# Kernel optimization log

Measured on AMD Instinct MI355X. Metric: run time of the kernel, lower is better.

## Reference

```python
import jax, jax.numpy as jnp
import numpy as np

# Graph sizes
B, N, E = 8, 512, 262144          # graphs, nodes/graph, total edges
ND, ED, GD = 128, 64, 32          # node, edge, glob feature dims
FIN = 2 * ND + ED                 # 320 = msg('sr') + existing edges
CTX = GD                          # ctxt_dim = 0, ctxt is globs only
H1, OUT = 256, 64                 # feat_net hidden / output (== ED for 'add' residual)
AH, NHEADS = 64, 4                # attn_net hidden / heads
HEAD = OUT // NHEADS              # 16
EPS = 1e-5


def setup_inputs() -> dict:
    key = jax.random.key(0)
    ks = jax.random.split(key, 12)
    nodes = jax.random.normal(ks[0], (B, N, ND), jnp.float32)
    edges0 = jax.random.normal(ks[1], (E, ED), jnp.float32)
    globs = jax.random.normal(ks[2], (B, GD), jnp.float32)
    batch_idx = jnp.sort(jax.random.randint(ks[3], (E,), 0, B, jnp.int32))
    send_idx = jax.random.randint(ks[4], (E,), 0, N, jnp.int32)
    recv_idx = jax.random.randint(ks[5], (E,), 0, N, jnp.int32)
    # LayerNorm params over feat_inpt_dim
    ln_g = jnp.ones((FIN,), jnp.float32)
    ln_b = jnp.zeros((FIN,), jnp.float32)
    # feat_net: 2-layer SiLU MLP, ctxt concatenated at the input
    W1 = 0.05 * jax.random.normal(ks[6], (FIN + CTX, H1), jnp.float32)
    b1 = jnp.zeros((H1,), jnp.float32)
    W2 = 0.05 * jax.random.normal(ks[7], (H1, OUT), jnp.float32)
    b2 = jnp.zeros((OUT,), jnp.float32)
    # attn_net: 2-layer SiLU MLP -> n_heads scores
    A1 = 0.05 * jax.random.normal(ks[8], (FIN + CTX, AH), jnp.float32)
    ab1 = jnp.zeros((AH,), jnp.float32)
    A2 = 0.05 * jax.random.normal(ks[9], (AH, NHEADS), jnp.float32)
    ab2 = jnp.zeros((NHEADS,), jnp.float32)
    return dict(nodes=nodes, edges0=edges0, globs=globs, ln_g=ln_g, ln_b=ln_b,
                W1=W1, b1=b1, W2=W2, b2=b2, A1=A1, ab1=ab1, A2=A2, ab2=ab2,
                batch_idx=batch_idx, send_idx=send_idx, recv_idx=recv_idx)


def reference(nodes, edges0, globs, ln_g, ln_b, W1, b1, W2, b2, A1, ab1, A2, ab2,
              batch_idx, send_idx, recv_idx):
    # Build messages: gather sender/receiver node feats per edge ('sr')
    send = nodes[batch_idx, send_idx]                      # [E, ND]
    recv = nodes[batch_idx, recv_idx]                      # [E, ND]
    feats = jnp.concatenate([edges0, send, recv], axis=-1)  # [E, FIN]
    # Pre-LN
    mu = feats.mean(-1, keepdims=True)
    var = feats.var(-1, keepdims=True)
    feats = (feats - mu) * jax.lax.rsqrt(var + EPS) * ln_g + ln_b
    # Broadcast per-graph globals to edges (ctxt_from_mask)
    x = jnp.concatenate([feats, globs[batch_idx]], axis=-1)  # [E, FIN+CTX]
    # Attention scores / sqrt(feat_outp_dim)
    a = (jax.nn.silu(x @ A1 + ab1) @ A2 + ab2) / np.sqrt(OUT)  # [E, NHEADS]
    # Segment softmax over the sender dim (group by (graph, receiver))
    seg = batch_idx * N + recv_idx
    nseg = B * N
    amax = jax.ops.segment_max(a, seg, num_segments=nseg)
    amax = jnp.where(jnp.isfinite(amax), amax, 0.0)
    ae = jnp.exp(a - amax[seg])
    denom = jax.ops.segment_sum(ae, seg, num_segments=nseg)
    attn = ae / denom[seg]                                  # [E, NHEADS]
    attn = jnp.repeat(attn, HEAD, axis=-1)                  # [E, OUT]
    # Edge feature update + additive residual
    new_edges = jax.nn.silu(x @ W1 + b1) @ W2 + b2 + edges0  # [E, OUT]
    # Attention-weighted scatter-sum pool over senders, zeros for isolated nodes
    pooled = jax.ops.segment_sum(new_edges * attn, seg, num_segments=nseg)
    pooled = pooled.reshape(B, N, OUT)
    return new_edges, pooled
```

## Files before the change

### kernel.cpp

```cpp
#include <hip/hip_runtime.h>
#include <hip/hip_bf16.h>
#include <cstdint>

typedef __bf16 bf16;
typedef __bf16 bf16x8 __attribute__((ext_vector_type(8)));
typedef float f32x4 __attribute__((ext_vector_type(4)));

#define E_TOT   262144
#define NNODE   512
#define NDIM    128
#define EDIM    64
#define GDIM    32
#define FIN     320
#define XD      352
#define H1D     256
#define OUTD    64
#define AHD     64
#define NHEADS  4
#define NSEG    4096
#define TE      48

#define SX_STR  360
#define SH_STR  264
#define SA_STR  72

#define PRM_LNG 0
#define PRM_LNB 320
#define PRM_B1  640
#define PRM_B2  896
#define PRM_A2  960
#define PRM_AB1 1216
#define PRM_AB2 1280
#define PRM_TOT 1284

#define SMEM_SX    0
#define SMEM_SA    25600
#define SMEM_SCORE 34560
#define SMEM_A2    35328
#define SMEM_LNG   36352
#define SMEM_LNB   37632
#define SMEM_IDX   38912
#define SMEM_TOT   39680

__device__ __forceinline__ float siluf(float v) {
    return v / (1.0f + __expf(-v));
}

__device__ __forceinline__ bool probe_bf16(const void* nodes, int t) {
    const unsigned short* u16 = (const unsigned short*)nodes;
    int lane = t & 63;
    int pl = 0;
    #pragma unroll
    for (int i = 0; i < 4; i++) {
        unsigned short u = u16[lane * 4 + i];
        int expo = (u >> 7) & 0xFF;
        pl += (((u & 0x7FFF) == 0) || (expo >= 97 && expo <= 137)) ? 1 : 0;
    }
    #pragma unroll
    for (int m = 1; m < 64; m <<= 1) pl += __shfl_xor(pl, m);
    return pl >= 240;
}

__global__ __launch_bounds__(256) void k_prep(
    const void* __restrict__ nodes,
    const void* __restrict__ W1, const void* __restrict__ W2, const void* __restrict__ A1,
    const void* __restrict__ ln_g, const void* __restrict__ ln_b,
    const void* __restrict__ b1, const void* __restrict__ b2,
    const void* __restrict__ A2, const void* __restrict__ ab1, const void* __restrict__ ab2,
    bf16* __restrict__ W1T, bf16* __restrict__ W2T, bf16* __restrict__ A1T,
    float* __restrict__ prm) {
    int b = blockIdx.x, t = threadIdx.x;
    bool isb = probe_bf16(nodes, t);
    if (b < 352) {
        int i = b * 256 + t;
        int k = i / H1D, n = i % H1D;
        float v = isb ? (float)((const bf16*)W1)[i] : ((const float*)W1)[i];
        W1T[n * XD + k] = (bf16)v;
    } else if (b < 416) {
        int i = (b - 352) * 256 + t;
        int k = i / OUTD, n = i % OUTD;
        float v = isb ? (float)((const bf16*)W2)[i] : ((const float*)W2)[i];
        W2T[n * H1D + k] = (bf16)v;
    } else if (b < 504) {
        int i = (b - 416) * 256 + t;
        int k = i / AHD, n = i % AHD;
        float v = isb ? (float)((const bf16*)A1)[i] : ((const float*)A1)[i];
        A1T[n * XD + k] = (bf16)v;
    } else {
        int i = (b - 504) * 256 + t;
        if (i < PRM_TOT) {
            const void* src; int off;
            if (i < 320)       { src = ln_g; off = i; }
            else if (i < 640)  { src = ln_b; off = i - 320; }
            else if (i < 896)  { src = b1;   off = i - 640; }
            else if (i < 960)  { src = b2;   off = i - 896; }
            else if (i < 1216) { src = A2;   off = i - 960; }
            else if (i < 1280) { src = ab1;  off = i - 1216; }
            else               { src = ab2;  off = i - 1280; }
            prm[i] = isb ? (float)((const bf16*)src)[off] : ((const float*)src)[off];
        }
    }
}

__global__ __launch_bounds__(256, 4) void k_edge(
    const void* __restrict__ nodes, const void* __restrict__ edges0,
    const void* __restrict__ globs, const float* __restrict__ prm,
    const int* __restrict__ bidx, const int* __restrict__ sidx,
    const int* __restrict__ ridx,
    const bf16* __restrict__ W1T, const bf16* __restrict__ W2T,
    const bf16* __restrict__ A1T,
    void* __restrict__ outNE, float* __restrict__ denom,
    float* __restrict__ pooled) {

    __shared__ __align__(16) char smem[SMEM_TOT];
    bf16*  sX    = (bf16*)(smem + SMEM_SX);
    bf16*  sH    = (bf16*)(smem + SMEM_SX);
    bf16*  sA    = (bf16*)(smem + SMEM_SA);
    float* sScore= (float*)(smem + SMEM_SCORE);
    float* sA2   = (float*)(smem + SMEM_A2);
    float* sLnG  = (float*)(smem + SMEM_LNG);
    float* sLnB  = (float*)(smem + SMEM_LNB);
    int*   sBi   = (int*)(smem + SMEM_IDX);
    int*   sSi   = sBi + TE;
    int*   sRi   = sBi + 2 * TE;
    int*   sSeg  = sBi + 3 * TE;

    const int t  = threadIdx.x;
    const int e0 = blockIdx.x * TE;
    const int ne = min(TE, E_TOT - e0);
    const bool isb = probe_bf16(nodes, t);

    if (t < TE) {
        int ge = e0 + t;
        if (t < ne) {
            int bi = bidx[ge], si = sidx[ge], ri = ridx[ge];
            sBi[t] = bi; sSi[t] = si; sRi[t] = ri;
            sSeg[t] = bi * NNODE + ri;
        } else {
            sBi[t] = 0; sSi[t] = 0; sRi[t] = 0; sSeg[t] = 0;
        }
    } else if (t < 128) {
        int c = t - 48;
        if (c < 80) ((float4*)sLnG)[c] = ((const float4*)(prm + PRM_LNG))[c];
    } else if (t < 208) {
        int c = t - 128;
        ((float4*)sLnB)[c] = ((const float4*)(prm + PRM_LNB))[c];
    } else {
        int c = t - 208;
        if (c < 32) {
            ((float4*)sA2)[c]      = ((const float4*)(prm + PRM_A2))[c];
            ((float4*)sA2)[c + 32] = ((const float4*)(prm + PRM_A2))[c + 32];
        }
    }
    __syncthreads();

    {
        const int eh = t >> 3, gl = t & 7;
        for (int half = 0; half < 2; half++) {
            const int e = half * 32 + eh;
            if (e >= TE) break;
            if (e >= ne) {
                bf16x8 zz = {};
                #pragma unroll
                for (int j = 0; j < 6; j++) {
                    int c = gl + j * 8;
                    if (c < 44) *(bf16x8*)&sX[e * SX_STR + c * 8] = zz;
                }
                continue;
            }
            const int ge = e0 + e;
            const int bi = sBi[e], si = sSi[e], ri = sRi[e];
            float v[40];
            #pragma unroll
            for (int j = 0; j < 5; j++) {
                const int c = gl + j * 8;
                const void* base; size_t off;
                if (c < 8)       { base = edges0; off = (size_t)ge * EDIM + c * 8; }
                else if (c < 24) { base = nodes;  off = (size_t)(bi * NNODE + si) * NDIM + (c - 8) * 8; }
                else             { base = nodes;  off = (size_t)(bi * NNODE + ri) * NDIM + (c - 24) * 8; }
                if (isb) {
                    bf16x8 x = *(const bf16x8*)((const bf16*)base + off);
                    #pragma unroll
                    for (int ii = 0; ii < 8; ii++) v[j * 8 + ii] = (float)x[ii];
                } else {
                    const float* sf = (const float*)base + off;
                    float4 f0 = ((const float4*)sf)[0];
                    float4 f1 = ((const float4*)sf)[1];
                    v[j*8+0]=f0.x; v[j*8+1]=f0.y; v[j*8+2]=f0.z; v[j*8+3]=f0.w;
                    v[j*8+4]=f1.x; v[j*8+5]=f1.y; v[j*8+6]=f1.z; v[j*8+7]=f1.w;
                }
            }
            float s = 0.f, sq = 0.f;
            #pragma unroll
            for (int ii = 0; ii < 40; ii++) { s += v[ii]; sq += v[ii] * v[ii]; }
            #pragma unroll
            for (int m = 1; m < 8; m <<= 1) { s += __shfl_xor(s, m); sq += __shfl_xor(sq, m); }
            float mean = s * (1.0f / FIN);
            float var  = sq * (1.0f / FIN) - mean * mean;
            float rstd = rsqrtf(var + 1e-5f);
            #pragma unroll
            for (int j = 0; j < 5; j++) {
                const int c = gl + j * 8;
                const float* gP = &sLnG[c * 8];
                const float* bP = &sLnB[c * 8];
                bf16x8 o;
                #pragma unroll
                for (int ii = 0; ii < 8; ii++)
                    o[ii] = (bf16)((v[j * 8 + ii] - mean) * rstd * gP[ii] + bP[ii]);
                *(bf16x8*)&sX[e * SX_STR + c * 8] = o;
            }
            if (gl < 4) {
                const int c = 40 + gl;
                size_t off = (size_t)bi * GDIM + gl * 8;
                bf16x8 o;
                if (isb) {
                    o = *(const bf16x8*)((const bf16*)globs + off);
                } else {
                    const float* sf = (const float*)globs + off;
                    float4 f0 = ((const float4*)sf)[0];
                    float4 f1 = ((const float4*)sf)[1];
                    o[0]=(bf16)f0.x; o[1]=(bf16)f0.y; o[2]=(bf16)f0.z; o[3]=(bf16)f0.w;
                    o[4]=(bf16)f1.x; o[5]=(bf16)f1.y; o[6]=(bf16)f1.z; o[7]=(bf16)f1.w;
                }
                *(bf16x8*)&sX[e * SX_STR + c * 8] = o;
            }
        }
    }
    __syncthreads();

    const int w = t >> 6, lane = t & 63, quad = lane >> 4, l15 = lane & 15;
    f32x4 z = {0.f, 0.f, 0.f, 0.f};

    f32x4 acc[3][4], accA[3];
    #pragma unroll
    for (int s2 = 0; s2 < 3; s2++) { accA[s2] = z; for (int i = 0; i < 4; i++) acc[s2][i] = z; }
    {
        const bf16* pW = W1T + (size_t)(w * 64 + l15) * XD + quad * 8;
        const bf16* pA = A1T + (size_t)(w * 16 + l15) * XD + quad * 8;
        bf16x8 bw[4], ba;
        #pragma unroll
        for (int i = 0; i < 4; i++) bw[i] = *(const bf16x8*)(pW + (size_t)i * 16 * XD);
        ba = *(const bf16x8*)pA;
        for (int kk = 0; kk < 11; kk++) {
            bf16x8 bwn[4], ban;
            if (kk < 10) {
                #pragma unroll
                for (int i = 0; i < 4; i++) bwn[i] = *(const bf16x8*)(pW + (size_t)i * 16 * XD + (kk + 1) * 32);
                ban = *(const bf16x8*)(pA + (kk + 1) * 32);
            }
            const int kc = kk * 32 + quad * 8;
            bf16x8 a[3];
            #pragma unroll
            for (int s2 = 0; s2 < 3; s2++) a[s2] = *(bf16x8*)&sX[(s2 * 16 + l15) * SX_STR + kc];
            #pragma unroll
            for (int i = 0; i < 4; i++)
                #pragma unroll
                for (int s2 = 0; s2 < 3; s2++)
                    acc[s2][i] = __builtin_amdgcn_mfma_f32_16x16x32_bf16(a[s2], bw[i], acc[s2][i], 0, 0, 0);
            #pragma unroll
            for (int s2 = 0; s2 < 3; s2++)
                accA[s2] = __builtin_amdgcn_mfma_f32_16x16x32_bf16(a[s2], ba, accA[s2], 0, 0, 0);
            if (kk < 10) {
                #pragma unroll
                for (int i = 0; i < 4; i++) bw[i] = bwn[i];
                ba = ban;
            }
        }
    }
    __syncthreads();

    #pragma unroll
    for (int i = 0; i < 4; i++) {
        const int n = w * 64 + i * 16 + l15;
        const float bb = prm[PRM_B1 + n];
        #pragma unroll
        for (int s2 = 0; s2 < 3; s2++)
            #pragma unroll
            for (int r = 0; r < 4; r++)
                sH[(s2 * 16 + quad * 4 + r) * SH_STR + n] = (bf16)siluf(acc[s2][i][r] + bb);
    }
    {
        const int n = w * 16 + l15;
        const float ba1 = prm[PRM_AB1 + n];
        #pragma unroll
        for (int s2 = 0; s2 < 3; s2++)
            #pragma unroll
            for (int r = 0; r < 4; r++)
                sA[(s2 * 16 + quad * 4 + r) * SA_STR + n] = (bf16)siluf(accA[s2][r] + ba1);
    }
    __syncthreads();

    if (t < TE * NHEADS) {
        const int e = t >> 2, h = t & 3;
        if (e < ne) {
            float dot = 0.f;
            #pragma unroll
            for (int c = 0; c < 8; c++) {
                bf16x8 v = *(bf16x8*)&sA[e * SA_STR + c * 8];
                #pragma unroll
                for (int ii = 0; ii < 8; ii++)
                    dot += (float)v[ii] * sA2[(c * 8 + ii) * NHEADS + h];
            }
            float ex = __expf((dot + prm[PRM_AB2 + h]) * 0.125f);
            sScore[e * 4 + h] = ex;
            atomicAdd(&denom[sSeg[e] * NHEADS + h], ex);
        }
    }
    __syncthreads();

    {
        f32x4 c2[3] = {z, z, z};
        const int n = w * 16 + l15;
        const bf16* pW2 = W2T + (size_t)n * H1D + quad * 8;
        bf16x8 b2f = *(const bf16x8*)pW2;
        for (int kk = 0; kk < 8; kk++) {
            bf16x8 b2n;
            if (kk < 7) b2n = *(const bf16x8*)(pW2 + (kk + 1) * 32);
            const int kc = kk * 32 + quad * 8;
            #pragma unroll
            for (int s2 = 0; s2 < 3; s2++) {
                bf16x8 a = *(bf16x8*)&sH[(s2 * 16 + l15) * SH_STR + kc];
                c2[s2] = __builtin_amdgcn_mfma_f32_16x16x32_bf16(a, b2f, c2[s2], 0, 0, 0);
            }
            if (kk < 7) b2f = b2n;
        }
        const float bb2 = prm[PRM_B2 + n];
        #pragma unroll
        for (int s2 = 0; s2 < 3; s2++)
            #pragma unroll
            for (int r = 0; r < 4; r++) {
                const int row = s2 * 16 + quad * 4 + r;
                if (row < ne) {
                    size_t off = (size_t)(e0 + row) * EDIM + n;
                    float ev = isb ? (float)((const bf16*)edges0)[off] : ((const float*)edges0)[off];
                    float v = c2[s2][r] + bb2 + ev;
                    if (isb) ((bf16*)outNE)[off] = (bf16)v;
                    else     ((float*)outNE)[off] = v;
                    float ex = sScore[row * 4 + w];
                    atomicAdd(&pooled[(size_t)sSeg[row] * OUTD + n], v * ex);
                }
            }
    }
}

__global__ __launch_bounds__(256) void k_norm(const float* __restrict__ pooled,
                                              const float* __restrict__ denom,
                                              const void* __restrict__ nodes,
                                              void* __restrict__ d_out) {
    int i = blockIdx.x * 256 + threadIdx.x;
    bool isb = probe_bf16(nodes, threadIdx.x);
    int s = i >> 6, j = i & 63, h = j >> 4;
    float den = denom[s * 4 + h];
    float v = (den > 0.f) ? pooled[i] / den : 0.0f;
    size_t po = (size_t)E_TOT * OUTD + i;
    if (isb) ((bf16*)d_out)[po] = (bf16)v;
    else     ((float*)d_out)[po] = v;
}

static char* align_up(char* p, size_t a) {
    return (char*)(((uintptr_t)p + (a - 1)) & ~(uintptr_t)(a - 1));
}

extern "C" void kernel_launch(void* const* d_in, const int* in_sizes, int n_in,
                              void* d_out, int out_size, void* d_ws, size_t ws_size,
                              hipStream_t stream) {
    const void* nodes  = d_in[0];
    const void* edges0 = d_in[1];
    const void* globs  = d_in[2];
    const void* ln_g   = d_in[3];
    const void* ln_b   = d_in[4];
    const void* W1     = d_in[5];
    const void* b1     = d_in[6];
    const void* W2     = d_in[7];
    const void* b2     = d_in[8];
    const void* A1     = d_in[9];
    const void* ab1    = d_in[10];
    const void* A2     = d_in[11];
    const void* ab2    = d_in[12];
    const int*  bidx   = (const int*)d_in[13];
    const int*  sidx   = (const int*)d_in[14];
    const int*  ridx   = (const int*)d_in[15];

    char* p = (char*)d_ws;
    float*    prm    = (float*)p;    p = align_up(p + PRM_TOT * 4, 256);
    bf16*     W1T    = (bf16*)p;     p = align_up(p + XD * H1D * 2, 256);
    bf16*     W2T    = (bf16*)p;     p = align_up(p + H1D * OUTD * 2, 256);
    bf16*     A1T    = (bf16*)p;     p = align_up(p + XD * AHD * 2, 256);
    float*    denom  = (float*)p;    p += NSEG * NHEADS * 4;
    float*    pooled = (float*)p;    p += (size_t)NSEG * OUTD * 4;

    hipMemsetAsync(denom, 0, NSEG * NHEADS * 4 + (size_t)NSEG * OUTD * 4, stream);
    k_prep<<<dim3(510), dim3(256), 0, stream>>>(
        nodes, W1, W2, A1, ln_g, ln_b, b1, b2, A2, ab1, ab2,
        W1T, W2T, A1T, prm);
    k_edge<<<dim3((E_TOT + TE - 1) / TE), dim3(256), 0, stream>>>(
        nodes, edges0, globs, prm,
        bidx, sidx, ridx, W1T, W2T, A1T, d_out, denom, pooled);
    k_norm<<<dim3(NSEG * OUTD / 256), dim3(256), 0, stream>>>(pooled, denom, nodes, d_out);
}
```

Baseline: 345.6 us.

## Shrink edge tile to 32, raise occupancy, fold zeroing into prep kernel

Reduces the edges per block from 48 to 32, which shrinks shared memory and lets the launch bound ask for 6 blocks per CU. Each thread now handles exactly one edge row in the gather/LayerNorm stage, and LN gamma/beta are read straight from global memory instead of being staged in shared memory. The memset is replaced by zeroing blocks appended to the prep kernel, MFMA loops drop their manual register prefetch and are wrapped in s_setprio, and the denominator atomics are moved to the end of the kernel. The trade-off is more blocks, with weights reloaded from global/L2 for each smaller tile, and the loss of the software prefetch.

New measurement: 385.8 us. 1.12x slower.

```diff
diff --git a/kernel.cpp b/kernel.cpp
--- a/kernel.cpp
+++ b/kernel.cpp
@@ -18,7 +18,7 @@
 #define AHD     64
 #define NHEADS  4
 #define NSEG    4096
-#define TE      48
+#define TE      32
 
 #define SX_STR  360
 #define SH_STR  264
@@ -34,16 +34,17 @@
 #define PRM_TOT 1284
 
 #define SMEM_SX    0
-#define SMEM_SA    25600
-#define SMEM_SCORE 34560
-#define SMEM_A2    35328
-#define SMEM_LNG   36352
-#define SMEM_LNB   37632
-#define SMEM_IDX   38912
-#define SMEM_TOT   39680
+#define SMEM_SA    16896
+#define SMEM_SCORE 23040
+#define SMEM_A2    23552
+#define SMEM_SEG   24576
+#define SMEM_TOT   24704
+
+#define ZOFF 510
+#define ZBLK 272
 
 __device__ __forceinline__ float siluf(float v) {
-    return v / (1.0f + __expf(-v));
+    return v * __builtin_amdgcn_rcpf(1.0f + __expf(-v));
 }
 
 __device__ __forceinline__ bool probe_bf16(const void* nodes, int t) {
@@ -68,8 +69,13 @@
     const void* __restrict__ b1, const void* __restrict__ b2,
     const void* __restrict__ A2, const void* __restrict__ ab1, const void* __restrict__ ab2,
     bf16* __restrict__ W1T, bf16* __restrict__ W2T, bf16* __restrict__ A1T,
-    float* __restrict__ prm) {
+    float* __restrict__ prm, float* __restrict__ denom) {
     int b = blockIdx.x, t = threadIdx.x;
+    if (b >= ZOFF) {
+        float4 z4 = {0.f, 0.f, 0.f, 0.f};
+        ((float4*)denom)[(b - ZOFF) * 256 + t] = z4;
+        return;
+    }
     bool isb = probe_bf16(nodes, t);
     if (b < 352) {
         int i = b * 256 + t;
@@ -102,7 +108,7 @@
     }
 }
 
-__global__ __launch_bounds__(256, 4) void k_edge(
+__global__ __launch_bounds__(256, 6) void k_edge(
     const void* __restrict__ nodes, const void* __restrict__ edges0,
     const void* __restrict__ globs, const float* __restrict__ prm,
     const int* __restrict__ bidx, const int* __restrict__ sidx,
@@ -118,112 +124,75 @@
     bf16*  sA    = (bf16*)(smem + SMEM_SA);
     float* sScore= (float*)(smem + SMEM_SCORE);
     float* sA2   = (float*)(smem + SMEM_A2);
-    float* sLnG  = (float*)(smem + SMEM_LNG);
-    float* sLnB  = (float*)(smem + SMEM_LNB);
-    int*   sBi   = (int*)(smem + SMEM_IDX);
-    int*   sSi   = sBi + TE;
-    int*   sRi   = sBi + 2 * TE;
-    int*   sSeg  = sBi + 3 * TE;
+    int*   sSeg  = (int*)(smem + SMEM_SEG);
 
     const int t  = threadIdx.x;
     const int e0 = blockIdx.x * TE;
-    const int ne = min(TE, E_TOT - e0);
     const bool isb = probe_bf16(nodes, t);
 
-    if (t < TE) {
-        int ge = e0 + t;
-        if (t < ne) {
-            int bi = bidx[ge], si = sidx[ge], ri = ridx[ge];
-            sBi[t] = bi; sSi[t] = si; sRi[t] = ri;
-            sSeg[t] = bi * NNODE + ri;
-        } else {
-            sBi[t] = 0; sSi[t] = 0; sRi[t] = 0; sSeg[t] = 0;
-        }
-    } else if (t < 128) {
-        int c = t - 48;
-        if (c < 80) ((float4*)sLnG)[c] = ((const float4*)(prm + PRM_LNG))[c];
-    } else if (t < 208) {
-        int c = t - 128;
-        ((float4*)sLnB)[c] = ((const float4*)(prm + PRM_LNB))[c];
-    } else {
-        int c = t - 208;
-        if (c < 32) {
-            ((float4*)sA2)[c]      = ((const float4*)(prm + PRM_A2))[c];
-            ((float4*)sA2)[c + 32] = ((const float4*)(prm + PRM_A2))[c + 32];
-        }
-    }
-    __syncthreads();
-
     {
+        if (t < 64) ((float4*)sA2)[t] = ((const float4*)(prm + PRM_A2))[t];
         const int eh = t >> 3, gl = t & 7;
-        for (int half = 0; half < 2; half++) {
-            const int e = half * 32 + eh;
-            if (e >= TE) break;
-            if (e >= ne) {
-                bf16x8 zz = {};
+        const int ge = e0 + eh;
+        const int bi = bidx[ge], si = sidx[ge], ri = ridx[ge];
+        if (gl == 0) sSeg[eh] = bi * NNODE + ri;
+        float v[40];
+        #pragma unroll
+        for (int j = 0; j < 5; j++) {
+            const int c = gl + j * 8;
+            const void* base; size_t off;
+            if (c < 8)       { base = edges0; off = (size_t)ge * EDIM + c * 8; }
+            else if (c < 24) { base = nodes;  off = (size_t)(bi * NNODE + si) * NDIM + (c - 8) * 8; }
+            else             { base = nodes;  off = (size_t)(bi * NNODE + ri) * NDIM + (c - 24) * 8; }
+            if (isb) {
+                bf16x8 x = *(const bf16x8*)((const bf16*)base + off);
                 #pragma unroll
-                for (int j = 0; j < 6; j++) {
-                    int c = gl + j * 8;
-                    if (c < 44) *(bf16x8*)&sX[e * SX_STR + c * 8] = zz;
-                }
-                continue;
-            }
-            const int ge = e0 + e;
-            const int bi = sBi[e], si = sSi[e], ri = sRi[e];
-            float v[40];
-            #pragma unroll
-            for (int j = 0; j < 5; j++) {
-                const int c = gl + j * 8;
-                const void* base; size_t off;
-                if (c < 8)       { base = edges0; off = (size_t)ge * EDIM + c * 8; }
-                else if (c < 24) { base = nodes;  off = (size_t)(bi * NNODE + si) * NDIM + (c - 8) * 8; }
-                else             { base = nodes;  off = (size_t)(bi * NNODE + ri) * NDIM + (c - 24) * 8; }
-                if (isb) {
-                    bf16x8 x = *(const bf16x8*)((const bf16*)base + off);
-                    #pragma unroll
-                    for (int ii = 0; ii < 8; ii++) v[j * 8 + ii] = (float)x[ii];
-                } else {
-                    const float* sf = (const float*)base + off;
-                    float4 f0 = ((const float4*)sf)[0];
-                    float4 f1 = ((const float4*)sf)[1];
-                    v[j*8+0]=f0.x; v[j*8+1]=f0.y; v[j*8+2]=f0.z; v[j*8+3]=f0.w;
-                    v[j*8+4]=f1.x; v[j*8+5]=f1.y; v[j*8+6]=f1.z; v[j*8+7]=f1.w;
-                }
-            }
-            float s = 0.f, sq = 0.f;
-            #pragma unroll
-            for (int ii = 0; ii < 40; ii++) { s += v[ii]; sq += v[ii] * v[ii]; }
-            #pragma unroll
-            for (int m = 1; m < 8; m <<= 1) { s += __shfl_xor(s, m); sq += __shfl_xor(sq, m); }
-            float mean = s * (1.0f / FIN);
-            float var  = sq * (1.0f / FIN) - mean * mean;
-            float rstd = rsqrtf(var + 1e-5f);
-            #pragma unroll
-            for (int j = 0; j < 5; j++) {
-                const int c = gl + j * 8;
-                const float* gP = &sLnG[c * 8];
-                const float* bP = &sLnB[c * 8];
-                bf16x8 o;
-                #pragma unroll
-                for (int ii = 0; ii < 8; ii++)
-                    o[ii] = (bf16)((v[j * 8 + ii] - mean) * rstd * gP[ii] + bP[ii]);
-                *(bf16x8*)&sX[e * SX_STR + c * 8] = o;
-            }
-            if (gl < 4) {
-                const int c = 40 + gl;
-                size_t off = (size_t)bi * GDIM + gl * 8;
-                bf16x8 o;
-                if (isb) {
-                    o = *(const bf16x8*)((const bf16*)globs + off);
-                } else {
-                    const float* sf = (const float*)globs + off;
-                    float4 f0 = ((const float4*)sf)[0];
-                    float4 f1 = ((const float4*)sf)[1];
-                    o[0]=(bf16)f0.x; o[1]=(bf16)f0.y; o[2]=(bf16)f0.z; o[3]=(bf16)f0.w;
-                    o[4]=(bf16)f1.x; o[5]=(bf16)f1.y; o[6]=(bf16)f1.z; o[7]=(bf16)f1.w;
-                }
-                *(bf16x8*)&sX[e * SX_STR + c * 8] = o;
-            }
+                for (int ii = 0; ii < 8; ii++) v[j * 8 + ii] = (float)x[ii];
+            } else {
+                const float* sf = (const float*)base + off;
+                float4 f0 = ((const float4*)sf)[0];
+                float4 f1 = ((const float4*)sf)[1];
+                v[j*8+0]=f0.x; v[j*8+1]=f0.y; v[j*8+2]=f0.z; v[j*8+3]=f0.w;
+                v[j*8+4]=f1.x; v[j*8+5]=f1.y; v[j*8+6]=f1.z; v[j*8+7]=f1.w;
+            }
+        }
+        float s = 0.f, sq = 0.f;
+        #pragma unroll
+        for (int ii = 0; ii < 40; ii++) { s += v[ii]; sq += v[ii] * v[ii]; }
+        #pragma unroll
+        for (int m = 1; m < 8; m <<= 1) { s += __shfl_xor(s, m); sq += __shfl_xor(sq, m); }
+        float mean = s * (1.0f / FIN);
+        float var  = sq * (1.0f / FIN) - mean * mean;
+        float rstd = rsqrtf(var + 1e-5f);
+        #pragma unroll
+        for (int j = 0; j < 5; j++) {
+            const int c = gl + j * 8;
+            float4 g0 = ((const float4*)(prm + PRM_LNG))[c * 2];
+            float4 g1 = ((const float4*)(prm + PRM_LNG))[c * 2 + 1];
+            float4 p0 = ((const float4*)(prm + PRM_LNB))[c * 2];
+            float4 p1 = ((const float4*)(prm + PRM_LNB))[c * 2 + 1];
+            float gg[8] = {g0.x, g0.y, g0.z, g0.w, g1.x, g1.y, g1.z, g1.w};
+            float pp[8] = {p0.x, p0.y, p0.z, p0.w, p1.x, p1.y, p1.z, p1.w};
+            bf16x8 o;
+            #pragma unroll
+            for (int ii = 0; ii < 8; ii++)
+                o[ii] = (bf16)((v[j * 8 + ii] - mean) * rstd * gg[ii] + pp[ii]);
+            *(bf16x8*)&sX[eh * SX_STR + c * 8] = o;
+        }
+        if (gl < 4) {
+            const int c = 40 + gl;
+            size_t off = (size_t)bi * GDIM + gl * 8;
+            bf16x8 o;
+            if (isb) {
+                o = *(const bf16x8*)((const bf16*)globs + off);
+            } else {
+                const float* sf = (const float*)globs + off;
+                float4 f0 = ((const float4*)sf)[0];
+                float4 f1 = ((const float4*)sf)[1];
+                o[0]=(bf16)f0.x; o[1]=(bf16)f0.y; o[2]=(bf16)f0.z; o[3]=(bf16)f0.w;
+                o[4]=(bf16)f1.x; o[5]=(bf16)f1.y; o[6]=(bf16)f1.z; o[7]=(bf16)f1.w;
+            }
+            *(bf16x8*)&sX[eh * SX_STR + c * 8] = o;
         }
     }
     __syncthreads();
@@ -231,40 +200,30 @@
     const int w = t >> 6, lane = t & 63, quad = lane >> 4, l15 = lane & 15;
     f32x4 z = {0.f, 0.f, 0.f, 0.f};
 
-    f32x4 acc[3][4], accA[3];
+    f32x4 acc[2][4], accA[2];
     #pragma unroll
-    for (int s2 = 0; s2 < 3; s2++) { accA[s2] = z; for (int i = 0; i < 4; i++) acc[s2][i] = z; }
+    for (int s2 = 0; s2 < 2; s2++) { accA[s2] = z; for (int i = 0; i < 4; i++) acc[s2][i] = z; }
     {
         const bf16* pW = W1T + (size_t)(w * 64 + l15) * XD + quad * 8;
         const bf16* pA = A1T + (size_t)(w * 16 + l15) * XD + quad * 8;
-        bf16x8 bw[4], ba;
-        #pragma unroll
-        for (int i = 0; i < 4; i++) bw[i] = *(const bf16x8*)(pW + (size_t)i * 16 * XD);
-        ba = *(const bf16x8*)pA;
         for (int kk = 0; kk < 11; kk++) {
-            bf16x8 bwn[4], ban;
-            if (kk < 10) {
-                #pragma unroll
-                for (int i = 0; i < 4; i++) bwn[i] = *(const bf16x8*)(pW + (size_t)i * 16 * XD + (kk + 1) * 32);
-                ban = *(const bf16x8*)(pA + (kk + 1) * 32);
-            }
+            bf16x8 bw[4], ba;
+            #pragma unroll
+            for (int i = 0; i < 4; i++)
+                bw[i] = *(const bf16x8*)(pW + (size_t)i * 16 * XD + kk * 32);
+            ba = *(const bf16x8*)(pA + kk * 32);
             const int kc = kk * 32 + quad * 8;
-            bf16x8 a[3];
-            #pragma unroll
-            for (int s2 = 0; s2 < 3; s2++) a[s2] = *(bf16x8*)&sX[(s2 * 16 + l15) * SX_STR + kc];
-            #pragma unroll
-            for (int i = 0; i < 4; i++)
-                #pragma unroll
-                for (int s2 = 0; s2 < 3; s2++)
-                    acc[s2][i] = __builtin_amdgcn_mfma_f32_16x16x32_bf16(a[s2], bw[i], acc[s2][i], 0, 0, 0);
-            #pragma unroll
-            for (int s2 = 0; s2 < 3; s2++)
-                accA[s2] = __builtin_amdgcn_mfma_f32_16x16x32_bf16(a[s2], ba, accA[s2], 0, 0, 0);
-            if (kk < 10) {
-                #pragma unroll
-                for (int i = 0; i < 4; i++) bw[i] = bwn[i];
-                ba = ban;
-            }
+            bf16x8 a0 = *(bf16x8*)&sX[l15 * SX_STR + kc];
+            bf16x8 a1 = *(bf16x8*)&sX[(16 + l15) * SX_STR + kc];
+            __builtin_amdgcn_s_setprio(1);
+            #pragma unroll
+            for (int i = 0; i < 4; i++) {
+                acc[0][i] = __builtin_amdgcn_mfma_f32_16x16x32_bf16(a0, bw[i], acc[0][i], 0, 0, 0);
+                acc[1][i] = __builtin_amdgcn_mfma_f32_16x16x32_bf16(a1, bw[i], acc[1][i], 0, 0, 0);
+            }
+            accA[0] = __builtin_amdgcn_mfma_f32_16x16x32_bf16(a0, ba, accA[0], 0, 0, 0);
+            accA[1] = __builtin_amdgcn_mfma_f32_16x16x32_bf16(a1, ba, accA[1], 0, 0, 0);
+            __builtin_amdgcn_s_setprio(0);
         }
     }
     __syncthreads();
@@ -274,7 +233,7 @@
         const int n = w * 64 + i * 16 + l15;
         const float bb = prm[PRM_B1 + n];
         #pragma unroll
-        for (int s2 = 0; s2 < 3; s2++)
+        for (int s2 = 0; s2 < 2; s2++)
             #pragma unroll
             for (int r = 0; r < 4; r++)
                 sH[(s2 * 16 + quad * 4 + r) * SH_STR + n] = (bf16)siluf(acc[s2][i][r] + bb);
@@ -283,7 +242,7 @@
         const int n = w * 16 + l15;
         const float ba1 = prm[PRM_AB1 + n];
         #pragma unroll
-        for (int s2 = 0; s2 < 3; s2++)
+        for (int s2 = 0; s2 < 2; s2++)
             #pragma unroll
             for (int r = 0; r < 4; r++)
                 sA[(s2 * 16 + quad * 4 + r) * SA_STR + n] = (bf16)siluf(accA[s2][r] + ba1);
@@ -292,54 +251,57 @@
 
     if (t < TE * NHEADS) {
         const int e = t >> 2, h = t & 3;
-        if (e < ne) {
-            float dot = 0.f;
-            #pragma unroll
-            for (int c = 0; c < 8; c++) {
-                bf16x8 v = *(bf16x8*)&sA[e * SA_STR + c * 8];
-                #pragma unroll
-                for (int ii = 0; ii < 8; ii++)
-                    dot += (float)v[ii] * sA2[(c * 8 + ii) * NHEADS + h];
-            }
-            float ex = __expf((dot + prm[PRM_AB2 + h]) * 0.125f);
-            sScore[e * 4 + h] = ex;
-            atomicAdd(&denom[sSeg[e] * NHEADS + h], ex);
-        }
+        float dot = 0.f;
+        #pragma unroll
+        for (int c = 0; c < 8; c++) {
+            bf16x8 vv = *(bf16x8*)&sA[e * SA_STR + c * 8];
+            #pragma unroll
+            for (int ii = 0; ii < 8; ii++)
+                dot += (float)vv[ii] * sA2[(c * 8 + ii) * NHEADS + h];
+        }
+        sScore[t] = __expf((dot + prm[PRM_AB2 + h]) * 0.125f);
     }
     __syncthreads();
 
     {
-        f32x4 c2[3] = {z, z, z};
+        f32x4 c2[2] = {z, z};
         const int n = w * 16 + l15;
-        const bf16* pW2 = W2T + (size_t)n * H1D + quad * 8;
-        bf16x8 b2f = *(const bf16x8*)pW2;
-        for (int kk = 0; kk < 8; kk++) {
-            bf16x8 b2n;
-            if (kk < 7) b2n = *(const bf16x8*)(pW2 + (kk + 1) * 32);
-            const int kc = kk * 32 + quad * 8;
-            #pragma unroll
-            for (int s2 = 0; s2 < 3; s2++) {
-                bf16x8 a = *(bf16x8*)&sH[(s2 * 16 + l15) * SH_STR + kc];
-                c2[s2] = __builtin_amdgcn_mfma_f32_16x16x32_bf16(a, b2f, c2[s2], 0, 0, 0);
-            }
-            if (kk < 7) b2f = b2n;
-        }
-        const float bb2 = prm[PRM_B2 + n];
-        #pragma unroll
-        for (int s2 = 0; s2 < 3; s2++)
+        float ev[2][4], sc[2][4];
+        #pragma unroll
+        for (int s2 = 0; s2 < 2; s2++)
             #pragma unroll
             for (int r = 0; r < 4; r++) {
                 const int row = s2 * 16 + quad * 4 + r;
-                if (row < ne) {
-                    size_t off = (size_t)(e0 + row) * EDIM + n;
-                    float ev = isb ? (float)((const bf16*)edges0)[off] : ((const float*)edges0)[off];
-                    float v = c2[s2][r] + bb2 + ev;
-                    if (isb) ((bf16*)outNE)[off] = (bf16)v;
-                    else     ((float*)outNE)[off] = v;
-                    float ex = sScore[row * 4 + w];
-                    atomicAdd(&pooled[(size_t)sSeg[row] * OUTD + n], v * ex);
-                }
-            }
+                size_t off = (size_t)(e0 + row) * EDIM + n;
+                ev[s2][r] = isb ? (float)((const bf16*)edges0)[off] : ((const float*)edges0)[off];
+                sc[s2][r] = sScore[row * 4 + w];
+            }
+        const bf16* pW2 = W2T + (size_t)n * H1D + quad * 8;
+        for (int kk = 0; kk < 8; kk++) {
+            bf16x8 b2f = *(const bf16x8*)(pW2 + kk * 32);
+            const int kc = kk * 32 + quad * 8;
+            bf16x8 a0 = *(bf16x8*)&sH[l15 * SH_STR + kc];
+            bf16x8 a1 = *(bf16x8*)&sH[(16 + l15) * SH_STR + kc];
+            __builtin_amdgcn_s_setprio(1);
+            c2[0] = __builtin_amdgcn_mfma_f32_16x16x32_bf16(a0, b2f, c2[0], 0, 0, 0);
+            c2[1] = __builtin_amdgcn_mfma_f32_16x16x32_bf16(a1, b2f, c2[1], 0, 0, 0);
+            __builtin_amdgcn_s_setprio(0);
+        }
+        const float bb2 = prm[PRM_B2 + n];
+        #pragma unroll
+        for (int s2 = 0; s2 < 2; s2++)
+            #pragma unroll
+            for (int r = 0; r < 4; r++) {
+                const int row = s2 * 16 + quad * 4 + r;
+                size_t off = (size_t)(e0 + row) * EDIM + n;
+                float v = c2[s2][r] + bb2 + ev[s2][r];
+                if (isb) ((bf16*)outNE)[off] = (bf16)v;
+                else     ((float*)outNE)[off] = v;
+                atomicAdd(&pooled[(size_t)sSeg[row] * OUTD + n], v * sc[s2][r]);
+            }
+    }
+    if (t < TE * NHEADS) {
+        atomicAdd(&denom[sSeg[t >> 2] * NHEADS + (t & 3)], sScore[t]);
     }
 }
 
@@ -389,11 +351,10 @@
     float*    denom  = (float*)p;    p += NSEG * NHEADS * 4;
     float*    pooled = (float*)p;    p += (size_t)NSEG * OUTD * 4;
 
-    hipMemsetAsync(denom, 0, NSEG * NHEADS * 4 + (size_t)NSEG * OUTD * 4, stream);
-    k_prep<<<dim3(510), dim3(256), 0, stream>>>(
+    k_prep<<<dim3(ZOFF + ZBLK), dim3(256), 0, stream>>>(
         nodes, W1, W2, A1, ln_g, ln_b, b1, b2, A2, ab1, ab2,
-        W1T, W2T, A1T, prm);
-    k_edge<<<dim3((E_TOT + TE - 1) / TE), dim3(256), 0, stream>>>(
+        W1T, W2T, A1T, prm, denom);
+    k_edge<<<dim3(E_TOT / TE), dim3(256), 0, stream>>>(
         nodes, edges0, globs, prm,
         bidx, sidx, ridx, W1T, W2T, A1T, d_out, denom, pooled);
     k_norm<<<dim3(NSEG * OUTD / 256), dim3(256), 0, stream>>>(pooled, denom, nodes, d_out);
```

## Fold LayerNorm affine into weights, fuse workspace zeroing into prep, nontemporal stores

Applied to the files above, without the earlier changes.

The LayerNorm gamma is folded into the rows of W1 and A1, and beta is folded into the biases b1 and ab1 during the prep kernel. The per-edge normalization therefore writes only (x-mean)*rstd and no longer stages ln_g/ln_b in shared memory. The hipMemsetAsync of denom and pooled is replaced by extra zeroing blocks inside k_prep, removing one launch. New-edge outputs use nontemporal stores to reduce cache pollution. Folding gamma into the weights before the bf16 cast slightly changes rounding.

Result: slower. 395.4 us (+14.4%).

```diff
diff --git a/kernel.cpp b/kernel.cpp
--- a/kernel.cpp
+++ b/kernel.cpp
@@ -24,26 +24,29 @@
 #define SH_STR  264
 #define SA_STR  72
 
-#define PRM_LNG 0
-#define PRM_LNB 320
-#define PRM_B1  640
-#define PRM_B2  896
-#define PRM_A2  960
-#define PRM_AB1 1216
-#define PRM_AB2 1280
-#define PRM_TOT 1284
+#define PRM_B1  0
+#define PRM_B2  256
+#define PRM_A2  320
+#define PRM_AB1 576
+#define PRM_AB2 640
+#define PRM_TOT 644
 
 #define SMEM_SX    0
 #define SMEM_SA    25600
 #define SMEM_SCORE 34560
 #define SMEM_A2    35328
-#define SMEM_LNG   36352
-#define SMEM_LNB   37632
-#define SMEM_IDX   38912
-#define SMEM_TOT   39680
+#define SMEM_IDX   36352
+#define SMEM_TOT   37120
+
+#define ZOFF 507
+#define ZBLK 272
 
 __device__ __forceinline__ float siluf(float v) {
     return v / (1.0f + __expf(-v));
+}
+
+__device__ __forceinline__ float ldf(const void* p, int i, bool isb) {
+    return isb ? (float)((const bf16*)p)[i] : ((const float*)p)[i];
 }
 
 __device__ __forceinline__ bool probe_bf16(const void* nodes, int t) {
@@ -68,37 +71,43 @@
     const void* __restrict__ b1, const void* __restrict__ b2,
     const void* __restrict__ A2, const void* __restrict__ ab1, const void* __restrict__ ab2,
     bf16* __restrict__ W1T, bf16* __restrict__ W2T, bf16* __restrict__ A1T,
-    float* __restrict__ prm) {
+    float* __restrict__ prm, float* __restrict__ denom) {
     int b = blockIdx.x, t = threadIdx.x;
+    if (b >= ZOFF) {
+        float4 z4 = {0.f, 0.f, 0.f, 0.f};
+        ((float4*)denom)[(b - ZOFF) * 256 + t] = z4;
+        return;
+    }
     bool isb = probe_bf16(nodes, t);
     if (b < 352) {
-        int i = b * 256 + t;
-        int k = i / H1D, n = i % H1D;
-        float v = isb ? (float)((const bf16*)W1)[i] : ((const float*)W1)[i];
-        W1T[n * XD + k] = (bf16)v;
+        int k = b, n = t;
+        float g = (k < FIN) ? ldf(ln_g, k, isb) : 1.0f;
+        W1T[n * XD + k] = (bf16)(ldf(W1, k * H1D + n, isb) * g);
     } else if (b < 416) {
         int i = (b - 352) * 256 + t;
-        int k = i / OUTD, n = i % OUTD;
-        float v = isb ? (float)((const bf16*)W2)[i] : ((const float*)W2)[i];
-        W2T[n * H1D + k] = (bf16)v;
+        int k = i >> 6, n = i & 63;
+        W2T[n * H1D + k] = (bf16)ldf(W2, i, isb);
     } else if (b < 504) {
         int i = (b - 416) * 256 + t;
-        int k = i / AHD, n = i % AHD;
-        float v = isb ? (float)((const bf16*)A1)[i] : ((const float*)A1)[i];
-        A1T[n * XD + k] = (bf16)v;
+        int k = i >> 6, n = i & 63;
+        float g = (k < FIN) ? ldf(ln_g, k, isb) : 1.0f;
+        A1T[n * XD + k] = (bf16)(ldf(A1, i, isb) * g);
+    } else if (b == 504) {
+        float acc = ldf(b1, t, isb);
+        #pragma unroll 4
+        for (int k = 0; k < FIN; k++) acc += ldf(ln_b, k, isb) * ldf(W1, k * H1D + t, isb);
+        prm[PRM_B1 + t] = acc;
+    } else if (b == 505) {
+        if (t < AHD) {
+            float acc = ldf(ab1, t, isb);
+            #pragma unroll 4
+            for (int k = 0; k < FIN; k++) acc += ldf(ln_b, k, isb) * ldf(A1, k * AHD + t, isb);
+            prm[PRM_AB1 + t] = acc;
+        }
     } else {
-        int i = (b - 504) * 256 + t;
-        if (i < PRM_TOT) {
-            const void* src; int off;
-            if (i < 320)       { src = ln_g; off = i; }
-            else if (i < 640)  { src = ln_b; off = i - 320; }
-            else if (i < 896)  { src = b1;   off = i - 640; }
-            else if (i < 960)  { src = b2;   off = i - 896; }
-            else if (i < 1216) { src = A2;   off = i - 960; }
-            else if (i < 1280) { src = ab1;  off = i - 1216; }
-            else               { src = ab2;  off = i - 1280; }
-            prm[i] = isb ? (float)((const bf16*)src)[off] : ((const float*)src)[off];
-        }
+        prm[PRM_A2 + t] = ldf(A2, t, isb);
+        if (t < 64) prm[PRM_B2 + t] = ldf(b2, t, isb);
+        if (t < 4)  prm[PRM_AB2 + t] = ldf(ab2, t, isb);
     }
 }
 
@@ -118,8 +127,6 @@
     bf16*  sA    = (bf16*)(smem + SMEM_SA);
     float* sScore= (float*)(smem + SMEM_SCORE);
     float* sA2   = (float*)(smem + SMEM_A2);
-    float* sLnG  = (float*)(smem + SMEM_LNG);
-    float* sLnB  = (float*)(smem + SMEM_LNB);
     int*   sBi   = (int*)(smem + SMEM_IDX);
     int*   sSi   = sBi + TE;
     int*   sRi   = sBi + 2 * TE;
@@ -139,18 +146,8 @@
         } else {
             sBi[t] = 0; sSi[t] = 0; sRi[t] = 0; sSeg[t] = 0;
         }
-    } else if (t < 128) {
-        int c = t - 48;
-        if (c < 80) ((float4*)sLnG)[c] = ((const float4*)(prm + PRM_LNG))[c];
-    } else if (t < 208) {
-        int c = t - 128;
-        ((float4*)sLnB)[c] = ((const float4*)(prm + PRM_LNB))[c];
-    } else {
-        int c = t - 208;
-        if (c < 32) {
-            ((float4*)sA2)[c]      = ((const float4*)(prm + PRM_A2))[c];
-            ((float4*)sA2)[c + 32] = ((const float4*)(prm + PRM_A2))[c + 32];
-        }
+    } else if (t >= 64 && t < 128) {
+        ((float4*)sA2)[t - 64] = ((const float4*)(prm + PRM_A2))[t - 64];
     }
     __syncthreads();
 
@@ -201,12 +198,10 @@
             #pragma unroll
             for (int j = 0; j < 5; j++) {
                 const int c = gl + j * 8;
-                const float* gP = &sLnG[c * 8];
-                const float* bP = &sLnB[c * 8];
                 bf16x8 o;
                 #pragma unroll
                 for (int ii = 0; ii < 8; ii++)
-                    o[ii] = (bf16)((v[j * 8 + ii] - mean) * rstd * gP[ii] + bP[ii]);
+                    o[ii] = (bf16)((v[j * 8 + ii] - mean) * rstd);
                 *(bf16x8*)&sX[e * SX_STR + c * 8] = o;
             }
             if (gl < 4) {
@@ -296,10 +291,10 @@
             float dot = 0.f;
             #pragma unroll
             for (int c = 0; c < 8; c++) {
-                bf16x8 v = *(bf16x8*)&sA[e * SA_STR + c * 8];
+                bf16x8 vv = *(bf16x8*)&sA[e * SA_STR + c * 8];
                 #pragma unroll
                 for (int ii = 0; ii < 8; ii++)
-                    dot += (float)v[ii] * sA2[(c * 8 + ii) * NHEADS + h];
+                    dot += (float)vv[ii] * sA2[(c * 8 + ii) * NHEADS + h];
             }
             float ex = __expf((dot + prm[PRM_AB2 + h]) * 0.125f);
             sScore[e * 4 + h] = ex;
@@ -334,8 +329,8 @@
                     size_t off = (size_t)(e0 + row) * EDIM + n;
                     float ev = isb ? (float)((const bf16*)edges0)[off] : ((const float*)edges0)[off];
                     float v = c2[s2][r] + bb2 + ev;
-                    if (isb) ((bf16*)outNE)[off] = (bf16)v;
-                    else     ((float*)outNE)[off] = v;
+                    if (isb) { bf16 bv = (bf16)v; __builtin_nontemporal_store(bv, &((bf16*)outNE)[off]); }
+                    else     { __builtin_nontemporal_store(v, &((float*)outNE)[off]); }
                     float ex = sScore[row * 4 + w];
                     atomicAdd(&pooled[(size_t)sSeg[row] * OUTD + n], v * ex);
                 }
@@ -389,10 +384,9 @@
     float*    denom  = (float*)p;    p += NSEG * NHEADS * 4;
     float*    pooled = (float*)p;    p += (size_t)NSEG * OUTD * 4;
 
-    hipMemsetAsync(denom, 0, NSEG * NHEADS * 4 + (size_t)NSEG * OUTD * 4, stream);
-    k_prep<<<dim3(510), dim3(256), 0, stream>>>(
+    k_prep<<<dim3(ZOFF + ZBLK), dim3(256), 0, stream>>>(
         nodes, W1, W2, A1, ln_g, ln_b, b1, b2, A2, ab1, ab2,
-        W1T, W2T, A1T, prm);
+        W1T, W2T, A1T, prm, denom);
     k_edge<<<dim3((E_TOT + TE - 1) / TE), dim3(256), 0, stream>>>(
         nodes, edges0, globs, prm,
         bidx, sidx, ridx, W1T, W2T, A1T, d_out, denom, pooled);
```

## Replace atomic scatter pooling with counting-sort segmented gather pooling

Applied to the files above, without the earlier changes.

Removes the per-element float atomics into pooled and denom from the edge kernel. Edges are instead bucketed by (graph, receiver) segment using a histogram, a prefix scan and a scatter, which yields a sorted order. The edge kernel now writes unnormalized attention scores to a workspace buffer. A new pool kernel has one wavefront per segment gather new_edges and scores, then normalize. This adds three small kernels plus extra global reads and writes of the score and order buffers in exchange for eliminating atomic contention. The single-block prefix kernel adds serial latency.

Result: slower. 382.4 us (+10.6%).

```diff
diff --git a/kernel.cpp b/kernel.cpp
--- a/kernel.cpp
+++ b/kernel.cpp
@@ -5,6 +5,7 @@
 typedef __bf16 bf16;
 typedef __bf16 bf16x8 __attribute__((ext_vector_type(8)));
 typedef float f32x4 __attribute__((ext_vector_type(4)));
+typedef unsigned int u32;
 
 #define E_TOT   262144
 #define NNODE   512
@@ -35,15 +36,20 @@
 
 #define SMEM_SX    0
 #define SMEM_SA    25600
-#define SMEM_SCORE 34560
-#define SMEM_A2    35328
-#define SMEM_LNG   36352
-#define SMEM_LNB   37632
-#define SMEM_IDX   38912
-#define SMEM_TOT   39680
+#define SMEM_A2    34560
+#define SMEM_LNG   35584
+#define SMEM_LNB   36864
+#define SMEM_IDX   38144
+#define SMEM_TOT   38720
+
+#define HOFF 510
 
 __device__ __forceinline__ float siluf(float v) {
     return v / (1.0f + __expf(-v));
+}
+
+__device__ __forceinline__ float ldf(const void* p, size_t i, bool isb) {
+    return isb ? (float)((const bf16*)p)[i] : ((const float*)p)[i];
 }
 
 __device__ __forceinline__ bool probe_bf16(const void* nodes, int t) {
@@ -67,9 +73,16 @@
     const void* __restrict__ ln_g, const void* __restrict__ ln_b,
     const void* __restrict__ b1, const void* __restrict__ b2,
     const void* __restrict__ A2, const void* __restrict__ ab1, const void* __restrict__ ab2,
+    const int* __restrict__ bidx, const int* __restrict__ ridx,
     bf16* __restrict__ W1T, bf16* __restrict__ W2T, bf16* __restrict__ A1T,
-    float* __restrict__ prm) {
+    float* __restrict__ prm, u32* __restrict__ hist) {
     int b = blockIdx.x, t = threadIdx.x;
+    if (b >= HOFF) {
+        int ge = (b - HOFF) * 256 + t;
+        int seg = bidx[ge] * NNODE + ridx[ge];
+        atomicAdd(&hist[seg], 1u);
+        return;
+    }
     bool isb = probe_bf16(nodes, t);
     if (b < 352) {
         int i = b * 256 + t;
@@ -102,6 +115,42 @@
     }
 }
 
+__global__ __launch_bounds__(256) void k_prefix(const u32* __restrict__ hist,
+                                                u32* __restrict__ offs,
+                                                u32* __restrict__ cursor) {
+    __shared__ u32 tot[256];
+    __shared__ u32 base[256];
+    int t = threadIdx.x;
+    u32 h[16], s = 0;
+    #pragma unroll
+    for (int j = 0; j < 16; j++) { h[j] = hist[t * 16 + j]; s += h[j]; }
+    tot[t] = s;
+    __syncthreads();
+    if (t == 0) {
+        u32 r = 0;
+        for (int i = 0; i < 256; i++) { base[i] = r; r += tot[i]; }
+    }
+    __syncthreads();
+    u32 r = base[t];
+    #pragma unroll
+    for (int j = 0; j < 16; j++) {
+        offs[t * 16 + j] = r;
+        cursor[t * 16 + j] = r;
+        r += h[j];
+    }
+    if (t == 255) offs[NSEG] = E_TOT;
+}
+
+__global__ __launch_bounds__(256) void k_scatter(const int* __restrict__ bidx,
+                                                 const int* __restrict__ ridx,
+                                                 u32* __restrict__ cursor,
+                                                 u32* __restrict__ order) {
+    int ge = blockIdx.x * 256 + threadIdx.x;
+    int seg = bidx[ge] * NNODE + ridx[ge];
+    u32 pos = atomicAdd(&cursor[seg], 1u);
+    order[pos] = (u32)ge;
+}
+
 __global__ __launch_bounds__(256, 4) void k_edge(
     const void* __restrict__ nodes, const void* __restrict__ edges0,
     const void* __restrict__ globs, const float* __restrict__ prm,
@@ -109,21 +158,18 @@
     const int* __restrict__ ridx,
     const bf16* __restrict__ W1T, const bf16* __restrict__ W2T,
     const bf16* __restrict__ A1T,
-    void* __restrict__ outNE, float* __restrict__ denom,
-    float* __restrict__ pooled) {
+    void* __restrict__ outNE, float* __restrict__ scrS) {
 
     __shared__ __align__(16) char smem[SMEM_TOT];
     bf16*  sX    = (bf16*)(smem + SMEM_SX);
     bf16*  sH    = (bf16*)(smem + SMEM_SX);
     bf16*  sA    = (bf16*)(smem + SMEM_SA);
-    float* sScore= (float*)(smem + SMEM_SCORE);
     float* sA2   = (float*)(smem + SMEM_A2);
     float* sLnG  = (float*)(smem + SMEM_LNG);
     float* sLnB  = (float*)(smem + SMEM_LNB);
     int*   sBi   = (int*)(smem + SMEM_IDX);
     int*   sSi   = sBi + TE;
     int*   sRi   = sBi + 2 * TE;
-    int*   sSeg  = sBi + 3 * TE;
 
     const int t  = threadIdx.x;
     const int e0 = blockIdx.x * TE;
@@ -133,11 +179,9 @@
     if (t < TE) {
         int ge = e0 + t;
         if (t < ne) {
-            int bi = bidx[ge], si = sidx[ge], ri = ridx[ge];
-            sBi[t] = bi; sSi[t] = si; sRi[t] = ri;
-            sSeg[t] = bi * NNODE + ri;
+            sBi[t] = bidx[ge]; sSi[t] = sidx[ge]; sRi[t] = ridx[ge];
         } else {
-            sBi[t] = 0; sSi[t] = 0; sRi[t] = 0; sSeg[t] = 0;
+            sBi[t] = 0; sSi[t] = 0; sRi[t] = 0;
         }
     } else if (t < 128) {
         int c = t - 48;
@@ -296,17 +340,14 @@
             float dot = 0.f;
             #pragma unroll
             for (int c = 0; c < 8; c++) {
-                bf16x8 v = *(bf16x8*)&sA[e * SA_STR + c * 8];
+                bf16x8 vv = *(bf16x8*)&sA[e * SA_STR + c * 8];
                 #pragma unroll
                 for (int ii = 0; ii < 8; ii++)
-                    dot += (float)v[ii] * sA2[(c * 8 + ii) * NHEADS + h];
-            }
-            float ex = __expf((dot + prm[PRM_AB2 + h]) * 0.125f);
-            sScore[e * 4 + h] = ex;
-            atomicAdd(&denom[sSeg[e] * NHEADS + h], ex);
-        }
-    }
-    __syncthreads();
+                    dot += (float)vv[ii] * sA2[(c * 8 + ii) * NHEADS + h];
+            }
+            scrS[(size_t)(e0 + e) * NHEADS + h] = __expf((dot + prm[PRM_AB2 + h]) * 0.125f);
+        }
+    }
 
     {
         f32x4 c2[3] = {z, z, z};
@@ -336,25 +377,48 @@
                     float v = c2[s2][r] + bb2 + ev;
                     if (isb) ((bf16*)outNE)[off] = (bf16)v;
                     else     ((float*)outNE)[off] = v;
-                    float ex = sScore[row * 4 + w];
-                    atomicAdd(&pooled[(size_t)sSeg[row] * OUTD + n], v * ex);
                 }
             }
     }
 }
 
-__global__ __launch_bounds__(256) void k_norm(const float* __restrict__ pooled,
-                                              const float* __restrict__ denom,
+__global__ __launch_bounds__(256) void k_pool(const u32* __restrict__ offs,
+                                              const u32* __restrict__ order,
+                                              const float* __restrict__ scrS,
                                               const void* __restrict__ nodes,
                                               void* __restrict__ d_out) {
-    int i = blockIdx.x * 256 + threadIdx.x;
-    bool isb = probe_bf16(nodes, threadIdx.x);
-    int s = i >> 6, j = i & 63, h = j >> 4;
-    float den = denom[s * 4 + h];
-    float v = (den > 0.f) ? pooled[i] / den : 0.0f;
-    size_t po = (size_t)E_TOT * OUTD + i;
-    if (isb) ((bf16*)d_out)[po] = (bf16)v;
-    else     ((float*)d_out)[po] = v;
+    const int t = threadIdx.x;
+    const bool isb = probe_bf16(nodes, t);
+    const int ws = blockIdx.x * 4 + (t >> 6);
+    const int lane = t & 63, h = lane >> 4;
+    const void* newE = d_out;
+
+    const u32 o0 = offs[ws], o1 = offs[ws + 1];
+    float acc = 0.f, dsum = 0.f;
+    u32 i = o0;
+    for (; i + 4 <= o1; i += 4) {
+        u32 ea = order[i], eb = order[i + 1], ec = order[i + 2], ed = order[i + 3];
+        float sa = scrS[(size_t)ea * NHEADS + h];
+        float sb = scrS[(size_t)eb * NHEADS + h];
+        float sc = scrS[(size_t)ec * NHEADS + h];
+        float sd = scrS[(size_t)ed * NHEADS + h];
+        float va = ldf(newE, (size_t)ea * EDIM + lane, isb);
+        float vb = ldf(newE, (size_t)eb * EDIM + lane, isb);
+        float vc = ldf(newE, (size_t)ec * EDIM + lane, isb);
+        float vd = ldf(newE, (size_t)ed * EDIM + lane, isb);
+        acc += va * sa + vb * sb + vc * sc + vd * sd;
+        dsum += sa + sb + sc + sd;
+    }
+    for (; i < o1; i++) {
+        u32 e = order[i];
+        float s = scrS[(size_t)e * NHEADS + h];
+        acc += ldf(newE, (size_t)e * EDIM + lane, isb) * s;
+        dsum += s;
+    }
+    float r = (dsum > 0.f) ? acc / dsum : 0.f;
+    size_t po = (size_t)E_TOT * OUTD + (size_t)ws * OUTD + lane;
+    if (isb) ((bf16*)d_out)[po] = (bf16)r;
+    else     ((float*)d_out)[po] = r;
 }
 
 static char* align_up(char* p, size_t a) {
@@ -382,19 +446,24 @@
     const int*  ridx   = (const int*)d_in[15];
 
     char* p = (char*)d_ws;
-    float*    prm    = (float*)p;    p = align_up(p + PRM_TOT * 4, 256);
-    bf16*     W1T    = (bf16*)p;     p = align_up(p + XD * H1D * 2, 256);
-    bf16*     W2T    = (bf16*)p;     p = align_up(p + H1D * OUTD * 2, 256);
-    bf16*     A1T    = (bf16*)p;     p = align_up(p + XD * AHD * 2, 256);
-    float*    denom  = (float*)p;    p += NSEG * NHEADS * 4;
-    float*    pooled = (float*)p;    p += (size_t)NSEG * OUTD * 4;
-
-    hipMemsetAsync(denom, 0, NSEG * NHEADS * 4 + (size_t)NSEG * OUTD * 4, stream);
-    k_prep<<<dim3(510), dim3(256), 0, stream>>>(
+    float* prm    = (float*)p;  p = align_up(p + PRM_TOT * 4, 256);
+    bf16*  W1T    = (bf16*)p;   p = align_up(p + XD * H1D * 2, 256);
+    bf16*  W2T    = (bf16*)p;   p = align_up(p + H1D * OUTD * 2, 256);
+    bf16*  A1T    = (bf16*)p;   p = align_up(p + XD * AHD * 2, 256);
+    u32*   hist   = (u32*)p;    p += NSEG * 4;
+    u32*   offs   = (u32*)p;    p = align_up(p + (NSEG + 1) * 4, 256);
+    u32*   cursor = (u32*)p;    p += NSEG * 4;
+    u32*   order  = (u32*)p;    p += (size_t)E_TOT * 4;
+    float* scrS   = (float*)p;  p += (size_t)E_TOT * NHEADS * 4;
+
+    hipMemsetAsync(hist, 0, NSEG * 4, stream);
+    k_prep<<<dim3(HOFF + E_TOT / 256), dim3(256), 0, stream>>>(
         nodes, W1, W2, A1, ln_g, ln_b, b1, b2, A2, ab1, ab2,
-        W1T, W2T, A1T, prm);
+        bidx, ridx, W1T, W2T, A1T, prm, hist);
+    k_prefix<<<dim3(1), dim3(256), 0, stream>>>(hist, offs, cursor);
+    k_scatter<<<dim3(E_TOT / 256), dim3(256), 0, stream>>>(bidx, ridx, cursor, order);
     k_edge<<<dim3((E_TOT + TE - 1) / TE), dim3(256), 0, stream>>>(
         nodes, edges0, globs, prm,
-        bidx, sidx, ridx, W1T, W2T, A1T, d_out, denom, pooled);
-    k_norm<<<dim3(NSEG * OUTD / 256), dim3(256), 0, stream>>>(pooled, denom, nodes, d_out);
-}
+        bidx, sidx, ridx, W1T, W2T, A1T, d_out, scrS);
+    k_pool<<<dim3(NSEG / 4), dim3(256), 0, stream>>>(offs, order, scrS, nodes, d_out);
+}
```
